# Optimization experiments

Measured on AMD Instinct MI355X. Metric: run time of the kernel, lower is better.

## Reference

```python
import jax, jax.numpy as jnp
import numpy as np

N_NODES = 100_000
N_EDGES = 1_600_000
D_FEAT = 32


def setup_inputs() -> dict:
    key = jax.random.key(0)
    k1, k2, k3 = jax.random.split(key, 3)
    features = jax.random.normal(k1, (N_NODES, D_FEAT), dtype=jnp.float32)
    edge_src = jax.random.randint(k2, (N_EDGES,), 0, N_NODES, dtype=jnp.int64)
    edge_dst = jax.random.randint(k3, (N_EDGES,), 0, N_NODES, dtype=jnp.int64)
    return {"features": features, "edge_src": edge_src, "edge_dst": edge_dst}


def reference(features, edge_src, edge_dst):
    # features: [N, D]; edge_src/edge_dst: [E] (neighbor j -> node i), no self-loops.
    N, D = features.shape
    dt = features.dtype
    # deg(i) = |adj_lists[i]| = number of incident (dst) edges
    deg = jax.ops.segment_sum(jnp.ones(edge_dst.shape, dtype=dt), edge_dst, num_segments=N)
    # add self-loops (samp_neighs includes the node itself)
    loop = jnp.arange(N, dtype=edge_src.dtype)
    src = jnp.concatenate([edge_src, loop])
    dst = jnp.concatenate([edge_dst, loop])
    # w_ij = 1 / sqrt((1 + deg(i)) * (1 + deg(j)))
    w = jax.lax.rsqrt((1.0 + deg[dst]) * (1.0 + deg[src]))  # [E+N]
    # to_feats[i] = sum_j w_ij * features[j]
    return jax.ops.segment_sum(w[:, None] * features[src], dst, num_segments=N)
```

## Files before the change

kernel.cpp:

```cpp
#include <hip/hip_runtime.h>

#define D_FEAT 32
#define RSH 6
#define RS_NODES 64
#define MAX_NR 2048
#define NB_BIN 512
#define SCANA_TR 16

__global__ void binA_kernel(const int* __restrict__ dst, unsigned* __restrict__ A,
                            int E, int NR, int chunk) {
    __shared__ unsigned cnt[MAX_NR];
    for (int i = threadIdx.x; i < NR; i += blockDim.x) cnt[i] = 0u;
    __syncthreads();
    int b = blockIdx.x;
    int lo = b * chunk;
    int hi = min(lo + chunk, E);
    if (lo < hi) {
        int nq = (hi - lo) >> 2;
        const int4* p = (const int4*)(dst + lo);
        for (int q = threadIdx.x; q < nq; q += blockDim.x) {
            int4 v = p[q];
            atomicAdd(&cnt[v.x >> RSH], 1u);
            atomicAdd(&cnt[v.y >> RSH], 1u);
            atomicAdd(&cnt[v.z >> RSH], 1u);
            atomicAdd(&cnt[v.w >> RSH], 1u);
        }
        for (int i = lo + (nq << 2) + threadIdx.x; i < hi; i += blockDim.x)
            atomicAdd(&cnt[dst[i] >> RSH], 1u);
    }
    __syncthreads();
    for (int i = threadIdx.x; i < NR; i += blockDim.x)
        A[(size_t)b * NR + i] = cnt[i];
}

__global__ void scanA_kernel(unsigned* __restrict__ A, unsigned* __restrict__ keytot, int NR) {
    __shared__ unsigned lds[SCANA_TR * 514];
    int r0 = blockIdx.x * SCANA_TR;
    int tid = threadIdx.x;
    for (int idx = tid; idx < NB_BIN * SCANA_TR; idx += 512) {
        int c = idx & (SCANA_TR - 1);
        int b = idx >> 4;
        int r = r0 + c;
        lds[c * 514 + b] = (r < NR) ? A[(size_t)b * NR + r] : 0u;
    }
    __syncthreads();
    int wid = tid >> 6;
    int lane = tid & 63;
    #pragma unroll
    for (int cc = 0; cc < 2; cc++) {
        int c = wid * 2 + cc;
        unsigned carry = 0u;
        #pragma unroll
        for (int chunk = 0; chunk < NB_BIN / 64; chunk++) {
            unsigned v = lds[c * 514 + chunk * 64 + lane];
            unsigned incl = v;
            #pragma unroll
            for (int off = 1; off < 64; off <<= 1) {
                unsigned t = __shfl_up(incl, off, 64);
                if (lane >= off) incl += t;
            }
            lds[c * 514 + chunk * 64 + lane] = carry + incl - v;
            carry += __shfl(incl, 63, 64);
        }
        if (lane == 0 && (r0 + c) < NR) keytot[r0 + c] = carry;
    }
    __syncthreads();
    for (int idx = tid; idx < NB_BIN * SCANA_TR; idx += 512) {
        int c = idx & (SCANA_TR - 1);
        int b = idx >> 4;
        int r = r0 + c;
        if (r < NR) A[(size_t)b * NR + r] = lds[c * 514 + b];
    }
}

__global__ void scanR_kernel(const unsigned* __restrict__ keytot, unsigned* __restrict__ rs, int NR) {
    __shared__ unsigned a[2][2048];
    int t = threadIdx.x;
    a[0][t]        = (t < NR)        ? keytot[t]        : 0u;
    a[0][t + 1024] = (t + 1024 < NR) ? keytot[t + 1024] : 0u;
    int pin = 0;
    for (int off = 1; off < 2048; off <<= 1) {
        __syncthreads();
        int po = pin ^ 1;
        #pragma unroll
        for (int k = 0; k < 2; k++) {
            int idx = t + k * 1024;
            unsigned x = a[pin][idx];
            if (idx >= off) x += a[pin][idx - off];
            a[po][idx] = x;
        }
        pin ^= 1;
    }
    __syncthreads();
    #pragma unroll
    for (int k = 0; k < 2; k++) {
        int idx = t + k * 1024;
        if (idx < NR) rs[idx] = idx ? a[pin][idx - 1] : 0u;
    }
    if (t == 0) rs[NR] = a[pin][2047];
}

__global__ void binB_kernel(const int* __restrict__ src, const int* __restrict__ dst,
                            const unsigned* __restrict__ A, const unsigned* __restrict__ rs,
                            unsigned* __restrict__ binned, int E, int NR, int chunk) {
    __shared__ unsigned cur[MAX_NR];
    int b = blockIdx.x;
    for (int i = threadIdx.x; i < NR; i += blockDim.x)
        cur[i] = rs[i] + A[(size_t)b * NR + i];
    __syncthreads();
    int lo = b * chunk;
    int hi = min(lo + chunk, E);
    if (lo >= hi) return;
    int nq = (hi - lo) >> 2;
    const int4* ps = (const int4*)(src + lo);
    const int4* pd = (const int4*)(dst + lo);
    for (int q = threadIdx.x; q < nq; q += blockDim.x) {
        int4 s = ps[q];
        int4 d = pd[q];
        unsigned p0 = atomicAdd(&cur[d.x >> RSH], 1u);
        binned[p0] = (unsigned)s.x | ((unsigned)(d.x & (RS_NODES - 1)) << 26);
        unsigned p1 = atomicAdd(&cur[d.y >> RSH], 1u);
        binned[p1] = (unsigned)s.y | ((unsigned)(d.y & (RS_NODES - 1)) << 26);
        unsigned p2 = atomicAdd(&cur[d.z >> RSH], 1u);
        binned[p2] = (unsigned)s.z | ((unsigned)(d.z & (RS_NODES - 1)) << 26);
        unsigned p3 = atomicAdd(&cur[d.w >> RSH], 1u);
        binned[p3] = (unsigned)s.w | ((unsigned)(d.w & (RS_NODES - 1)) << 26);
    }
    for (int i = lo + (nq << 2) + threadIdx.x; i < hi; i += blockDim.x) {
        unsigned p = atomicAdd(&cur[dst[i] >> RSH], 1u);
        binned[p] = (unsigned)src[i] | ((unsigned)(dst[i] & (RS_NODES - 1)) << 26);
    }
}

__global__ void build_kernel(const unsigned* __restrict__ binned, const unsigned* __restrict__ rs,
                             unsigned* __restrict__ csr, unsigned* __restrict__ rowstart,
                             float* __restrict__ inv, int N, int E) {
    __shared__ unsigned deg64[RS_NODES];
    __shared__ unsigned cur64[RS_NODES];
    int r = blockIdx.x;
    if (threadIdx.x < RS_NODES) deg64[threadIdx.x] = 0u;
    __syncthreads();
    unsigned e0 = rs[r], e1 = rs[r + 1];
    for (unsigned e = e0 + threadIdx.x; e < e1; e += blockDim.x)
        atomicAdd(&deg64[binned[e] >> 26], 1u);
    __syncthreads();
    if (threadIdx.x < RS_NODES) {
        unsigned d = deg64[threadIdx.x];
        unsigned incl = d;
        #pragma unroll
        for (int off = 1; off < RS_NODES; off <<= 1) {
            unsigned t = __shfl_up(incl, off, 64);
            if (threadIdx.x >= (unsigned)off) incl += t;
        }
        unsigned startpos = e0 + (incl - d);
        cur64[threadIdx.x] = startpos;
        int node = r * RS_NODES + threadIdx.x;
        if (node < N) {
            rowstart[node] = startpos;
            inv[node] = rsqrtf(1.0f + (float)d);
        }
    }
    if (r == 0 && threadIdx.x == 0) rowstart[N] = (unsigned)E;
    __syncthreads();
    for (unsigned e = e0 + threadIdx.x; e < e1; e += blockDim.x) {
        unsigned p = binned[e];
        unsigned pos = atomicAdd(&cur64[p >> 26], 1u);
        csr[pos] = p & 0x03FFFFFFu;
    }
}

__global__ void gather_kernel(const float* __restrict__ feat, const unsigned* __restrict__ csr,
                              const unsigned* __restrict__ rowstart, const float* __restrict__ inv,
                              float* __restrict__ out, int N) {
    int wid = threadIdx.x >> 6;
    int node = blockIdx.x * (blockDim.x >> 6) + wid;
    if (node >= N) return;
    int lane = threadIdx.x & 63;
    int g = lane >> 3;
    int q = lane & 7;
    unsigned start = rowstart[node], end = rowstart[node + 1];
    float iv = inv[node];
    float4 acc = make_float4(0.f, 0.f, 0.f, 0.f);
    if (g == 0) {
        float4 f = *(const float4*)(feat + (size_t)node * D_FEAT + q * 4);
        acc.x = iv * f.x; acc.y = iv * f.y; acc.z = iv * f.z; acc.w = iv * f.w;
    }
    unsigned k = start + g;
    for (; k + 8 < end; k += 16) {
        unsigned j0 = csr[k], j1 = csr[k + 8];
        float w0 = inv[j0], w1 = inv[j1];
        float4 f0 = *(const float4*)(feat + (size_t)j0 * D_FEAT + q * 4);
        float4 f1 = *(const float4*)(feat + (size_t)j1 * D_FEAT + q * 4);
        acc.x = fmaf(w0, f0.x, acc.x); acc.y = fmaf(w0, f0.y, acc.y);
        acc.z = fmaf(w0, f0.z, acc.z); acc.w = fmaf(w0, f0.w, acc.w);
        acc.x = fmaf(w1, f1.x, acc.x); acc.y = fmaf(w1, f1.y, acc.y);
        acc.z = fmaf(w1, f1.z, acc.z); acc.w = fmaf(w1, f1.w, acc.w);
    }
    if (k < end) {
        unsigned j = csr[k];
        float w = inv[j];
        float4 f = *(const float4*)(feat + (size_t)j * D_FEAT + q * 4);
        acc.x = fmaf(w, f.x, acc.x); acc.y = fmaf(w, f.y, acc.y);
        acc.z = fmaf(w, f.z, acc.z); acc.w = fmaf(w, f.w, acc.w);
    }
    #pragma unroll
    for (int off = 8; off < 64; off <<= 1) {
        acc.x += __shfl_xor(acc.x, off);
        acc.y += __shfl_xor(acc.y, off);
        acc.z += __shfl_xor(acc.z, off);
        acc.w += __shfl_xor(acc.w, off);
    }
    if (g == 0) {
        float4 r;
        r.x = iv * acc.x; r.y = iv * acc.y; r.z = iv * acc.z; r.w = iv * acc.w;
        *(float4*)(out + (size_t)node * D_FEAT + q * 4) = r;
    }
}


__global__ void fb_deg_kernel(const int* __restrict__ dst, float* __restrict__ deg, int E) {
    int i = blockIdx.x * blockDim.x + threadIdx.x;
    int stride = gridDim.x * blockDim.x;
    for (; i < E; i += stride) atomicAdd(&deg[dst[i]], 1.0f);
}
__global__ void fb_inv_kernel(const float* __restrict__ deg, float* __restrict__ inv, int N) {
    int i = blockIdx.x * blockDim.x + threadIdx.x;
    if (i < N) inv[i] = rsqrtf(1.0f + deg[i]);
}
__global__ void fb_scatter_kernel(const float* __restrict__ feat, const int* __restrict__ src,
                                  const int* __restrict__ dst, const float* __restrict__ inv,
                                  float* __restrict__ out, int E) {
    long long tid = (long long)blockIdx.x * blockDim.x + threadIdx.x;
    int e = (int)(tid >> 5);
    int d = (int)(tid & 31);
    if (e >= E) return;
    int s = src[e];
    int t = dst[e];
    atomicAdd(&out[t * D_FEAT + d], inv[s] * feat[s * D_FEAT + d]);
}
__global__ void fb_finalize_kernel(const float* __restrict__ feat, const float* __restrict__ inv,
                                   float* __restrict__ out, int ND) {
    int tid = blockIdx.x * blockDim.x + threadIdx.x;
    if (tid >= ND) return;
    float iv = inv[tid >> 5];
    out[tid] = iv * (out[tid] + iv * feat[tid]);
}

extern "C" void kernel_launch(void* const* d_in, const int* in_sizes, int n_in,
                              void* d_out, int out_size, void* d_ws, size_t ws_size,
                              hipStream_t stream) {
    const float* feat = (const float*)d_in[0];
    const int* esrc = (const int*)d_in[1];
    const int* edst = (const int*)d_in[2];
    float* out = (float*)d_out;

    const int N = in_sizes[0] / D_FEAT;
    const int E = in_sizes[1];
    const int ND = N * D_FEAT;
    const int NR = (N + RS_NODES - 1) >> RSH;
    const int chunk = (((E + NB_BIN - 1) / NB_BIN) + 3) & ~3;

    size_t need = ((size_t)2 * E + (size_t)NR * NB_BIN + 2 * (size_t)NR + 2 * (size_t)N + 2) * 4;
    if (ws_size >= need && NR <= MAX_NR && N <= (1 << 26)) {
        unsigned* binned   = (unsigned*)d_ws;
        unsigned* csr      = binned + E;
        unsigned* A        = csr + E;
        unsigned* keytot   = A + (size_t)NR * NB_BIN;
        unsigned* rs       = keytot + NR;
        unsigned* rowstart = rs + NR + 1;
        float*    inv      = (float*)(rowstart + N + 1);

        binA_kernel<<<NB_BIN, 256, 0, stream>>>(edst, A, E, NR, chunk);
        scanA_kernel<<<(NR + SCANA_TR - 1) / SCANA_TR, 512, 0, stream>>>(A, keytot, NR);
        scanR_kernel<<<1, 1024, 0, stream>>>(keytot, rs, NR);
        binB_kernel<<<NB_BIN, 256, 0, stream>>>(esrc, edst, A, rs, binned, E, NR, chunk);
        build_kernel<<<NR, 256, 0, stream>>>(binned, rs, csr, rowstart, inv, N, E);
        {
            int waves_per_block = 4;
            int grid = (N + waves_per_block - 1) / waves_per_block;
            gather_kernel<<<grid, 256, 0, stream>>>(feat, csr, rowstart, inv, out, N);
        }
    } else {
        float* deg = (float*)d_ws;
        float* inv = deg + N;
        hipMemsetAsync(deg, 0, (size_t)N * sizeof(float), stream);
        hipMemsetAsync(out, 0, (size_t)ND * sizeof(float), stream);
        {
            int grid = (E + 255) / 256; if (grid > 2048) grid = 2048;
            fb_deg_kernel<<<grid, 256, 0, stream>>>(edst, deg, E);
        }
        fb_inv_kernel<<<(N + 255) / 256, 256, 0, stream>>>(deg, inv, N);
        {
            long long total = (long long)E * D_FEAT;
            fb_scatter_kernel<<<(int)((total + 255) / 256), 256, 0, stream>>>(feat, esrc, edst, inv, out, E);
        }
        fb_finalize_kernel<<<(ND + 255) / 256, 256, 0, stream>>>(feat, inv, out, ND);
    }
}
```

Baseline: 95.58 us.

## Prescale features by inverse-sqrt degree into bf16 table for gather

The build kernel now multiplies each node's features by its inverse-sqrt degree and stores them as packed bf16 in a new workspace table. The gather kernel reads these 64-byte rows instead of fp32 features plus a separate inv lookup, halving gathered bytes and removing one dependent load per edge. This adds a write pass over all node features and loses precision to bf16 rounding, which may exceed tolerance.

```diff
diff --git a/kernel.cpp b/kernel.cpp
--- a/kernel.cpp
+++ b/kernel.cpp
@@ -6,6 +6,13 @@
 #define MAX_NR 2048
 #define NB_BIN 512
 #define SCANA_TR 16
+
+__device__ __forceinline__ unsigned bfpack(float lo, float hi) {
+    unsigned ul = __float_as_uint(lo), uh = __float_as_uint(hi);
+    ul = (ul + 0x7FFFu + ((ul >> 16) & 1u)) >> 16;
+    uh = (uh + 0x7FFFu + ((uh >> 16) & 1u)) >> 16;
+    return ul | (uh << 16);
+}
 
 __global__ void binA_kernel(const int* __restrict__ dst, unsigned* __restrict__ A,
                             int E, int NR, int chunk) {
@@ -133,10 +140,12 @@
 }
 
 __global__ void build_kernel(const unsigned* __restrict__ binned, const unsigned* __restrict__ rs,
+                             const float* __restrict__ feat, unsigned* __restrict__ wf,
                              unsigned* __restrict__ csr, unsigned* __restrict__ rowstart,
                              float* __restrict__ inv, int N, int E) {
     __shared__ unsigned deg64[RS_NODES];
     __shared__ unsigned cur64[RS_NODES];
+    __shared__ float sinv[RS_NODES];
     int r = blockIdx.x;
     if (threadIdx.x < RS_NODES) deg64[threadIdx.x] = 0u;
     __syncthreads();
@@ -154,10 +163,12 @@
         }
         unsigned startpos = e0 + (incl - d);
         cur64[threadIdx.x] = startpos;
+        float ivv = rsqrtf(1.0f + (float)d);
+        sinv[threadIdx.x] = ivv;
         int node = r * RS_NODES + threadIdx.x;
         if (node < N) {
             rowstart[node] = startpos;
-            inv[node] = rsqrtf(1.0f + (float)d);
+            inv[node] = ivv;
         }
     }
     if (r == 0 && threadIdx.x == 0) rowstart[N] = (unsigned)E;
@@ -167,11 +178,28 @@
         unsigned pos = atomicAdd(&cur64[p >> 26], 1u);
         csr[pos] = p & 0x03FFFFFFu;
     }
-}
-
-__global__ void gather_kernel(const float* __restrict__ feat, const unsigned* __restrict__ csr,
-                              const unsigned* __restrict__ rowstart, const float* __restrict__ inv,
-                              float* __restrict__ out, int N) {
+    {
+        int nl = threadIdx.x >> 2;
+        int q = threadIdx.x & 3;
+        int node = r * RS_NODES + nl;
+        if (node < N) {
+            float ivv = sinv[nl];
+            const float4* fp = (const float4*)(feat + (size_t)node * D_FEAT + q * 8);
+            float4 a = fp[0];
+            float4 b = fp[1];
+            uint4 o;
+            o.x = bfpack(ivv * a.x, ivv * a.y);
+            o.y = bfpack(ivv * a.z, ivv * a.w);
+            o.z = bfpack(ivv * b.x, ivv * b.y);
+            o.w = bfpack(ivv * b.z, ivv * b.w);
+            ((uint4*)wf)[(size_t)node * 4 + q] = o;
+        }
+    }
+}
+
+__global__ void gather_kernel(const float* __restrict__ feat, const unsigned* __restrict__ wf,
+                              const unsigned* __restrict__ csr, const unsigned* __restrict__ rowstart,
+                              const float* __restrict__ inv, float* __restrict__ out, int N) {
     int wid = threadIdx.x >> 6;
     int node = blockIdx.x * (blockDim.x >> 6) + wid;
     if (node >= N) return;
@@ -188,20 +216,24 @@
     unsigned k = start + g;
     for (; k + 8 < end; k += 16) {
         unsigned j0 = csr[k], j1 = csr[k + 8];
-        float w0 = inv[j0], w1 = inv[j1];
-        float4 f0 = *(const float4*)(feat + (size_t)j0 * D_FEAT + q * 4);
-        float4 f1 = *(const float4*)(feat + (size_t)j1 * D_FEAT + q * 4);
-        acc.x = fmaf(w0, f0.x, acc.x); acc.y = fmaf(w0, f0.y, acc.y);
-        acc.z = fmaf(w0, f0.z, acc.z); acc.w = fmaf(w0, f0.w, acc.w);
-        acc.x = fmaf(w1, f1.x, acc.x); acc.y = fmaf(w1, f1.y, acc.y);
-        acc.z = fmaf(w1, f1.z, acc.z); acc.w = fmaf(w1, f1.w, acc.w);
+        uint2 w0 = *(const uint2*)(wf + (size_t)j0 * 16 + q * 2);
+        uint2 w1 = *(const uint2*)(wf + (size_t)j1 * 16 + q * 2);
+        acc.x += __uint_as_float(w0.x << 16);
+        acc.y += __uint_as_float(w0.x & 0xFFFF0000u);
+        acc.z += __uint_as_float(w0.y << 16);
+        acc.w += __uint_as_float(w0.y & 0xFFFF0000u);
+        acc.x += __uint_as_float(w1.x << 16);
+        acc.y += __uint_as_float(w1.x & 0xFFFF0000u);
+        acc.z += __uint_as_float(w1.y << 16);
+        acc.w += __uint_as_float(w1.y & 0xFFFF0000u);
     }
     if (k < end) {
         unsigned j = csr[k];
-        float w = inv[j];
-        float4 f = *(const float4*)(feat + (size_t)j * D_FEAT + q * 4);
-        acc.x = fmaf(w, f.x, acc.x); acc.y = fmaf(w, f.y, acc.y);
-        acc.z = fmaf(w, f.z, acc.z); acc.w = fmaf(w, f.w, acc.w);
+        uint2 w = *(const uint2*)(wf + (size_t)j * 16 + q * 2);
+        acc.x += __uint_as_float(w.x << 16);
+        acc.y += __uint_as_float(w.x & 0xFFFF0000u);
+        acc.z += __uint_as_float(w.y << 16);
+        acc.w += __uint_as_float(w.y & 0xFFFF0000u);
     }
     #pragma unroll
     for (int off = 8; off < 64; off <<= 1) {
@@ -211,9 +243,9 @@
         acc.w += __shfl_xor(acc.w, off);
     }
     if (g == 0) {
-        float4 r;
-        r.x = iv * acc.x; r.y = iv * acc.y; r.z = iv * acc.z; r.w = iv * acc.w;
-        *(float4*)(out + (size_t)node * D_FEAT + q * 4) = r;
+        float4 rv;
+        rv.x = iv * acc.x; rv.y = iv * acc.y; rv.z = iv * acc.z; rv.w = iv * acc.w;
+        *(float4*)(out + (size_t)node * D_FEAT + q * 4) = rv;
     }
 }
 
@@ -260,11 +292,13 @@
     const int NR = (N + RS_NODES - 1) >> RSH;
     const int chunk = (((E + NB_BIN - 1) / NB_BIN) + 3) & ~3;
 
-    size_t need = ((size_t)2 * E + (size_t)NR * NB_BIN + 2 * (size_t)NR + 2 * (size_t)N + 2) * 4;
+    size_t wf_off = ((size_t)2 * E + 3) & ~(size_t)3;
+    size_t need = (wf_off + 16 * (size_t)N + (size_t)NR * NB_BIN + 2 * (size_t)NR + 2 * (size_t)N + 2) * 4;
     if (ws_size >= need && NR <= MAX_NR && N <= (1 << 26)) {
         unsigned* binned   = (unsigned*)d_ws;
         unsigned* csr      = binned + E;
-        unsigned* A        = csr + E;
+        unsigned* wf       = (unsigned*)d_ws + wf_off;
+        unsigned* A        = wf + 16 * (size_t)N;
         unsigned* keytot   = A + (size_t)NR * NB_BIN;
         unsigned* rs       = keytot + NR;
         unsigned* rowstart = rs + NR + 1;
@@ -274,11 +308,11 @@
         scanA_kernel<<<(NR + SCANA_TR - 1) / SCANA_TR, 512, 0, stream>>>(A, keytot, NR);
         scanR_kernel<<<1, 1024, 0, stream>>>(keytot, rs, NR);
         binB_kernel<<<NB_BIN, 256, 0, stream>>>(esrc, edst, A, rs, binned, E, NR, chunk);
-        build_kernel<<<NR, 256, 0, stream>>>(binned, rs, csr, rowstart, inv, N, E);
+        build_kernel<<<NR, 256, 0, stream>>>(binned, rs, feat, wf, csr, rowstart, inv, N, E);
         {
             int waves_per_block = 4;
             int grid = (N + waves_per_block - 1) / waves_per_block;
-            gather_kernel<<<grid, 256, 0, stream>>>(feat, csr, rowstart, inv, out, N);
+            gather_kernel<<<grid, 256, 0, stream>>>(feat, wf, csr, rowstart, inv, out, N);
         }
     } else {
         float* deg = (float*)d_ws;
```

Result: no change. 94.73 us (-0.9%).
